# Kernel tuning notes

Measured on AMD Instinct MI355X. Metric: run time of the kernel, lower is better.

Reference implementation:

```python
import jax, jax.numpy as jnp
import numpy as np

DIM = 256; H = 64; W = 64; NH = 8; NL = 1; NP = 8; HD = DIM // NH
B = 4


def _bilinear(img, grid):
    """torch.grid_sample(mode='bilinear', padding='zeros', align_corners=False).
    img: [C, Hl, Wl]; grid: [N, P, 2] normalized xy in [-1, 1]. Returns [C, N, P]."""
    Hl, Wl = img.shape[1], img.shape[2]
    x = (grid[..., 0] + 1.0) * (Wl * 0.5) - 0.5
    y = (grid[..., 1] + 1.0) * (Hl * 0.5) - 0.5
    x0 = jnp.floor(x); y0 = jnp.floor(y)
    wx = x - x0; wy = y - y0

    def gather(xi, yi):
        valid = (xi >= 0) & (xi < Wl) & (yi >= 0) & (yi < Hl)
        xc = jnp.clip(xi, 0, Wl - 1).astype(jnp.int32)
        yc = jnp.clip(yi, 0, Hl - 1).astype(jnp.int32)
        return img[:, yc, xc] * valid.astype(img.dtype)[None]  # [C, N, P]

    v00 = gather(x0, y0); v01 = gather(x0 + 1, y0)
    v10 = gather(x0, y0 + 1); v11 = gather(x0 + 1, y0 + 1)
    top = v00 * (1.0 - wx) + v01 * wx
    bot = v10 * (1.0 - wx) + v11 * wx
    return top * (1.0 - wy) + bot * wy


def _msda(value, loc, att):
    """multi_scale_deformable_attn_pytorch.
    value: [b, nv, NH, HD]; loc: [b, nq, NH, NL, NP, 2] in [0,1]; att: [b, nq, NH, NL, NP]."""
    b, nv, _, _ = value.shape
    nq = loc.shape[1]
    grids = 2.0 * loc - 1.0
    bn = b * NH
    level_shapes = [(H, W)] * NL  # all levels share the single [H, W] grid here
    sampled_levels = []
    offset = 0
    for l, (Hl, Wl) in enumerate(level_shapes):
        vl = value[:, offset:offset + Hl * Wl]                     # [b, HW, NH, HD]
        offset += Hl * Wl
        vl = vl.transpose(0, 2, 3, 1).reshape(bn, HD, Hl, Wl)      # [b*NH, HD, Hl, Wl]
        gl = grids[:, :, :, l].transpose(0, 2, 1, 3, 4).reshape(bn, nq, NP, 2)
        sampled_levels.append(jax.vmap(_bilinear)(vl, gl))         # [b*NH, HD, nq, NP]
    sampled = jnp.stack(sampled_levels, axis=3)                    # [b*NH, HD, nq, NL, NP]
    w = att.transpose(0, 2, 1, 3, 4).reshape(bn, 1, nq, NL, NP)
    out = jnp.sum(sampled * w, axis=(3, 4))                        # [b*NH, HD, nq]
    return out.reshape(b, NH, HD, nq).transpose(0, 3, 1, 2).reshape(b, nq, NH * HD)


def _forward(query, value, W_loc, b_loc, W_att, b_att, W_val, b_val, W_out, b_out):
    b = query.shape[0]
    nq = H * W
    q = query.transpose(0, 2, 3, 1).reshape(b, nq, DIM)
    v = value.transpose(0, 2, 3, 1).reshape(b, nq, DIM)
    loc = (q @ W_loc.T + b_loc).reshape(b, nq, NH, NL, NP, 2)
    att = jax.nn.softmax((q @ W_att.T + b_att).reshape(b, nq, NH, NL * NP), axis=-1)
    att = att.reshape(b, nq, NH, NL, NP)
    v = (v @ W_val.T + b_val).reshape(b, nq, NH, HD)
    out = _msda(v, loc, att)                                       # [b, nq, DIM]
    return out @ W_out.T + b_out


def setup_inputs() -> dict:
    key = jax.random.key(0)
    ks = jax.random.split(key, 12)
    s = 0.02
    return {
        "query": jax.random.normal(ks[0], (B, DIM, H, W), jnp.float32),
        "value": jax.random.normal(ks[1], (B, DIM, H, W), jnp.float32),
        "W_loc": jax.random.normal(ks[2], (NH * NL * NP * 2, DIM), jnp.float32) * s,
        "b_loc": jax.random.normal(ks[3], (NH * NL * NP * 2,), jnp.float32) * s,
        "W_att": jax.random.normal(ks[4], (NH * NL * NP, DIM), jnp.float32) * s,
        "b_att": jax.random.normal(ks[5], (NH * NL * NP,), jnp.float32) * s,
        "W_val": jax.random.normal(ks[6], (DIM, DIM), jnp.float32) * s,
        "b_val": jax.random.normal(ks[7], (DIM,), jnp.float32) * s,
        "W_out": jax.random.normal(ks[8], (DIM, DIM), jnp.float32) * s,
        "b_out": jax.random.normal(ks[9], (DIM,), jnp.float32) * s,
    }


def reference(query, value, W_loc, b_loc, W_att, b_att, W_val, b_val, W_out, b_out):
    return _forward(query, value, W_loc, b_loc, W_att, b_att, W_val, b_val, W_out, b_out)
```

## Files before the change

### kernel.cpp

```cpp
#include <hip/hip_runtime.h>
#include <hip/hip_bf16.h>
#include <math.h>

#define NQ   4096
#define DIMC 256
#define NHC  8
#define NPC  8
#define HDC  32
#define HC   64
#define WC   64
#define BC   4
#define LSTR 40

typedef __bf16 bf16x8 __attribute__((ext_vector_type(8)));
typedef __attribute__((ext_vector_type(4))) float f4;
typedef __attribute__((ext_vector_type(8))) short s8v;

__device__ __forceinline__ ushort f2bf(float f) {
  __hip_bfloat16 h = __float2bfloat16(f);
  union { __hip_bfloat16 h; ushort u; } c; c.h = h; return c.u;
}
__device__ __forceinline__ float bfu2f(ushort u) {
  union { unsigned i; float f; } c; c.i = ((unsigned)u) << 16; return c.f;
}
__device__ __forceinline__ float bflo(unsigned u) {
  union { unsigned i; float f; } c; c.i = u << 16; return c.f;
}
__device__ __forceinline__ float bfhi(unsigned u) {
  union { unsigned i; float f; } c; c.i = u & 0xffff0000u; return c.f;
}

__global__ __launch_bounds__(256) void k_locatt(
    const float* __restrict__ query,
    const float* __restrict__ W_loc, const float* __restrict__ b_loc,
    const float* __restrict__ W_att, const float* __restrict__ b_att,
    float* __restrict__ loc, float* __restrict__ att) {
  __shared__ __align__(16) ushort Ah[64 * LSTR], Al[64 * LSTR];
  __shared__ __align__(16) ushort Wh[64 * LSTR], Wl[64 * LSTR];
  const int b = blockIdx.z, n0 = blockIdx.x * 64, o0 = blockIdx.y * 64;
  const int tid = threadIdx.x, lane = tid & 63, wid = tid >> 6;
  const int wn0 = (wid & 1) * 32, wo0 = (wid >> 1) * 32;
  const int am = lane & 15, kq = (lane >> 4) * 8;
  const int an = tid & 63, ak = (tid >> 6) * 8;
  const int wo = tid >> 2, wk = (tid & 3) * 8;
  const float* Xb = query + (size_t)b * DIMC * NQ + n0 + an;
  const int oo = o0 + wo;
  const float* Wrow = (oo < 128) ? (W_loc + (size_t)oo * DIMC)
                                 : (W_att + (size_t)(oo - 128) * DIMC);

  f4 acc[2][2];
#pragma unroll
  for (int mi = 0; mi < 2; ++mi) { acc[mi][0] = (f4)0.f; acc[mi][1] = (f4)0.f; }

  float ax[8];
  float4 wx0, wx1;
#pragma unroll
  for (int j = 0; j < 8; ++j) ax[j] = Xb[(size_t)(ak + j) * NQ];
  wx0 = *(const float4*)(Wrow + wk);
  wx1 = *(const float4*)(Wrow + wk + 4);

  for (int t = 0; t < 8; ++t) {
    __syncthreads();
    {
      union { ushort u[8]; s8v s; } ph, pl;
#pragma unroll
      for (int j = 0; j < 8; ++j) {
        ushort h = f2bf(ax[j]);
        ph.u[j] = h;
        pl.u[j] = f2bf(ax[j] - bfu2f(h));
      }
      *(s8v*)(&Ah[an * LSTR + ak]) = ph.s;
      *(s8v*)(&Al[an * LSTR + ak]) = pl.s;
      float wt[8] = {wx0.x, wx0.y, wx0.z, wx0.w, wx1.x, wx1.y, wx1.z, wx1.w};
      union { ushort u[8]; s8v s; } qh, ql;
#pragma unroll
      for (int j = 0; j < 8; ++j) {
        ushort h = f2bf(wt[j]);
        qh.u[j] = h;
        ql.u[j] = f2bf(wt[j] - bfu2f(h));
      }
      *(s8v*)(&Wh[wo * LSTR + wk]) = qh.s;
      *(s8v*)(&Wl[wo * LSTR + wk]) = ql.s;
    }
    if (t < 7) {
      const int k0 = (t + 1) * 32;
#pragma unroll
      for (int j = 0; j < 8; ++j) ax[j] = Xb[(size_t)(k0 + ak + j) * NQ];
      wx0 = *(const float4*)(Wrow + k0 + wk);
      wx1 = *(const float4*)(Wrow + k0 + wk + 4);
    }
    __syncthreads();
    bf16x8 ah[2], al[2], bh[2], bl[2];
#pragma unroll
    for (int mi = 0; mi < 2; ++mi) {
      ah[mi] = *(const bf16x8*)(&Ah[(wn0 + mi * 16 + am) * LSTR + kq]);
      al[mi] = *(const bf16x8*)(&Al[(wn0 + mi * 16 + am) * LSTR + kq]);
    }
#pragma unroll
    for (int oj = 0; oj < 2; ++oj) {
      bh[oj] = *(const bf16x8*)(&Wh[(wo0 + oj * 16 + am) * LSTR + kq]);
      bl[oj] = *(const bf16x8*)(&Wl[(wo0 + oj * 16 + am) * LSTR + kq]);
    }
#pragma unroll
    for (int mi = 0; mi < 2; ++mi)
#pragma unroll
      for (int oj = 0; oj < 2; ++oj) {
        acc[mi][oj] = __builtin_amdgcn_mfma_f32_16x16x32_bf16(ah[mi], bh[oj], acc[mi][oj], 0, 0, 0);
        acc[mi][oj] = __builtin_amdgcn_mfma_f32_16x16x32_bf16(al[mi], bh[oj], acc[mi][oj], 0, 0, 0);
        acc[mi][oj] = __builtin_amdgcn_mfma_f32_16x16x32_bf16(ah[mi], bl[oj], acc[mi][oj], 0, 0, 0);
      }
  }
  const bool isAtt = (o0 >= 128);
  float* dstBase = isAtt ? att : loc;
  const float* bias = isAtt ? b_att : b_loc;
  const int ostride = isAtt ? 64 : 128;
  const int ob = isAtt ? o0 - 128 : o0;
#pragma unroll
  for (int oj = 0; oj < 2; ++oj) {
    const int o = ob + wo0 + oj * 16 + am;
    const float bv = bias[o];
#pragma unroll
    for (int mi = 0; mi < 2; ++mi) {
      const int nb = n0 + wn0 + mi * 16 + (lane >> 4) * 4;
#pragma unroll
      for (int r = 0; r < 4; ++r)
        dstBase[((size_t)b * NQ + nb + r) * ostride + o] = acc[mi][oj][r] + bv;
    }
  }
}

__global__ __launch_bounds__(256) void k_vproj(
    const float* __restrict__ value, const float* __restrict__ W_val,
    const float* __restrict__ b_val, ushort* __restrict__ vproj) {
  __shared__ __align__(16) ushort As[64 * LSTR];
  __shared__ __align__(16) ushort Ws[64 * LSTR];
  const int b = blockIdx.z, n0 = blockIdx.x * 64, o0 = blockIdx.y * 64;
  const int tid = threadIdx.x, lane = tid & 63, wid = tid >> 6;
  const int wn0 = (wid & 1) * 32, wo0 = (wid >> 1) * 32;
  const int am = lane & 15, kq = (lane >> 4) * 8;
  const int an = tid & 63, ak = (tid >> 6) * 8;
  const int wo = tid >> 2, wk = (tid & 3) * 8;
  const float* Xb = value + (size_t)b * DIMC * NQ + n0 + an;
  const float* Wrow = W_val + (size_t)(o0 + wo) * DIMC;

  f4 acc[2][2];
#pragma unroll
  for (int mi = 0; mi < 2; ++mi) { acc[mi][0] = (f4)0.f; acc[mi][1] = (f4)0.f; }

  float ax[8];
  float4 wx0, wx1;
#pragma unroll
  for (int j = 0; j < 8; ++j) ax[j] = Xb[(size_t)(ak + j) * NQ];
  wx0 = *(const float4*)(Wrow + wk);
  wx1 = *(const float4*)(Wrow + wk + 4);

  for (int t = 0; t < 8; ++t) {
    __syncthreads();
    {
      union { ushort u[8]; s8v s; } pa;
#pragma unroll
      for (int j = 0; j < 8; ++j) pa.u[j] = f2bf(ax[j]);
      *(s8v*)(&As[an * LSTR + ak]) = pa.s;
      float wt[8] = {wx0.x, wx0.y, wx0.z, wx0.w, wx1.x, wx1.y, wx1.z, wx1.w};
      union { ushort u[8]; s8v s; } pw;
#pragma unroll
      for (int j = 0; j < 8; ++j) pw.u[j] = f2bf(wt[j]);
      *(s8v*)(&Ws[wo * LSTR + wk]) = pw.s;
    }
    if (t < 7) {
      const int k0 = (t + 1) * 32;
#pragma unroll
      for (int j = 0; j < 8; ++j) ax[j] = Xb[(size_t)(k0 + ak + j) * NQ];
      wx0 = *(const float4*)(Wrow + k0 + wk);
      wx1 = *(const float4*)(Wrow + k0 + wk + 4);
    }
    __syncthreads();
    bf16x8 af[2], bf[2];
#pragma unroll
    for (int mi = 0; mi < 2; ++mi)
      af[mi] = *(const bf16x8*)(&As[(wn0 + mi * 16 + am) * LSTR + kq]);
#pragma unroll
    for (int oj = 0; oj < 2; ++oj)
      bf[oj] = *(const bf16x8*)(&Ws[(wo0 + oj * 16 + am) * LSTR + kq]);
#pragma unroll
    for (int mi = 0; mi < 2; ++mi)
#pragma unroll
      for (int oj = 0; oj < 2; ++oj)
        acc[mi][oj] = __builtin_amdgcn_mfma_f32_16x16x32_bf16(af[mi], bf[oj], acc[mi][oj], 0, 0, 0);
  }
#pragma unroll
  for (int oj = 0; oj < 2; ++oj) {
    const int o = o0 + wo0 + oj * 16 + am;
    const int h = o >> 5, d = o & 31;
    const float bias = b_val[o];
    ushort* dst = vproj + ((size_t)(b * NHC + h) * NQ) * HDC + d;
#pragma unroll
    for (int mi = 0; mi < 2; ++mi) {
      const int nb = n0 + wn0 + mi * 16 + (lane >> 4) * 4;
#pragma unroll
      for (int r = 0; r < 4; ++r)
        dst[(size_t)(nb + r) * HDC] = f2bf(acc[mi][oj][r] + bias);
    }
  }
}

__global__ __launch_bounds__(256) void k_sample(
    const float* __restrict__ loc, const float* __restrict__ attL,
    const ushort* __restrict__ vproj, ushort* __restrict__ msda) {
  __shared__ float4 Lc[64][9];
  __shared__ int4   Lo[64][9];
  const int b = blockIdx.z, h = blockIdx.y;
  const int tid = threadIdx.x;
  const int n0 = blockIdx.x * 64;
#pragma unroll
  for (int it = 0; it < 2; ++it) {
    const int idx = it * 256 + tid;
    const int q = idx >> 3, p = idx & 7;
    const int n = n0 + q;
    const float lg = attL[((size_t)b * NQ + n) * 64 + h * 8 + p];
    float m = lg;
#pragma unroll
    for (int off = 1; off < 8; off <<= 1) m = fmaxf(m, __shfl_xor(m, off, 64));
    const float e = __expf(lg - m);
    float s = e;
#pragma unroll
    for (int off = 1; off < 8; off <<= 1) s += __shfl_xor(s, off, 64);
    const float w = e / s;
    const float2 xy = *(const float2*)(loc + ((size_t)b * NQ + n) * 128 + h * 16 + p * 2);
    const float x = xy.x * 64.0f - 0.5f;
    const float y = xy.y * 64.0f - 0.5f;
    const float x0f = floorf(x), y0f = floorf(y);
    const float wx = x - x0f, wy = y - y0f;
    const int x0 = (int)x0f, y0 = (int)y0f;
    const int x1 = x0 + 1, y1 = y0 + 1;
    const float fx0 = (x0 >= 0 && x0 < WC) ? 1.f : 0.f;
    const float fx1 = (x1 >= 0 && x1 < WC) ? 1.f : 0.f;
    const float fy0 = (y0 >= 0 && y0 < HC) ? 1.f : 0.f;
    const float fy1 = (y1 >= 0 && y1 < HC) ? 1.f : 0.f;
    const int cx0 = min(max(x0, 0), WC - 1), cx1 = min(max(x1, 0), WC - 1);
    const int cy0 = min(max(y0, 0), HC - 1), cy1 = min(max(y1, 0), HC - 1);
    float4 cf;
    cf.x = w * (1.f - wx) * (1.f - wy) * fx0 * fy0;
    cf.y = w * wx * (1.f - wy) * fx1 * fy0;
    cf.z = w * (1.f - wx) * wy * fx0 * fy1;
    cf.w = w * wx * wy * fx1 * fy1;
    int4 of;
    of.x = (cy0 * WC + cx0) * HDC; of.y = (cy0 * WC + cx1) * HDC;
    of.z = (cy1 * WC + cx0) * HDC; of.w = (cy1 * WC + cx1) * HDC;
    Lc[q][p] = cf; Lo[q][p] = of;
  }
  __syncthreads();
  const int q = tid >> 2, d8 = (tid & 3) * 8;
  const int n = n0 + q;
  const ushort* vb = vproj + (size_t)((b * NHC + h) * NQ) * HDC + d8;
  float a[8] = {};
#pragma unroll
  for (int p = 0; p < 8; ++p) {
    const int4 of = Lo[q][p];
    const float4 cf = Lc[q][p];
    const uint4 u00 = *(const uint4*)(vb + of.x);
    const uint4 u01 = *(const uint4*)(vb + of.y);
    const uint4 u10 = *(const uint4*)(vb + of.z);
    const uint4 u11 = *(const uint4*)(vb + of.w);
    const unsigned c00[4] = {u00.x, u00.y, u00.z, u00.w};
    const unsigned c01[4] = {u01.x, u01.y, u01.z, u01.w};
    const unsigned c10[4] = {u10.x, u10.y, u10.z, u10.w};
    const unsigned c11[4] = {u11.x, u11.y, u11.z, u11.w};
#pragma unroll
    for (int j = 0; j < 4; ++j) {
      a[2 * j]     += cf.x * bflo(c00[j]) + cf.y * bflo(c01[j]) + cf.z * bflo(c10[j]) + cf.w * bflo(c11[j]);
      a[2 * j + 1] += cf.x * bfhi(c00[j]) + cf.y * bfhi(c01[j]) + cf.z * bfhi(c10[j]) + cf.w * bfhi(c11[j]);
    }
  }
  union { ushort u[8]; s8v s; } r;
#pragma unroll
  for (int j = 0; j < 8; ++j) r.u[j] = f2bf(a[j]);
  *(s8v*)(msda + ((size_t)b * NQ + n) * DIMC + h * HDC + d8) = r.s;
}

__global__ __launch_bounds__(256) void k_out(
    const ushort* __restrict__ msda, const float* __restrict__ W_out,
    const float* __restrict__ b_out, float* __restrict__ out) {
  __shared__ __align__(16) ushort As[64 * LSTR];
  __shared__ __align__(16) ushort Ws[64 * LSTR];
  const int b = blockIdx.z, n0 = blockIdx.x * 64, o0 = blockIdx.y * 64;
  const int tid = threadIdx.x, lane = tid & 63, wid = tid >> 6;
  const int wn0 = (wid & 1) * 32, wo0 = (wid >> 1) * 32;
  const int am = lane & 15, kq = (lane >> 4) * 8;
  const int ar = tid >> 2, akq = (tid & 3) * 8;
  const int wo = tid >> 2, wk = (tid & 3) * 8;
  const ushort* Ab = msda + ((size_t)b * NQ + n0 + ar) * DIMC + akq;
  const float* Wrow = W_out + (size_t)(o0 + wo) * DIMC;

  f4 acc[2][2];
#pragma unroll
  for (int mi = 0; mi < 2; ++mi) { acc[mi][0] = (f4)0.f; acc[mi][1] = (f4)0.f; }

  s8v aval = *(const s8v*)(Ab);
  float4 wx0 = *(const float4*)(Wrow + wk);
  float4 wx1 = *(const float4*)(Wrow + wk + 4);

  for (int t = 0; t < 8; ++t) {
    __syncthreads();
    *(s8v*)(&As[ar * LSTR + akq]) = aval;
    {
      float wt[8] = {wx0.x, wx0.y, wx0.z, wx0.w, wx1.x, wx1.y, wx1.z, wx1.w};
      union { ushort u[8]; s8v s; } pw;
#pragma unroll
      for (int j = 0; j < 8; ++j) pw.u[j] = f2bf(wt[j]);
      *(s8v*)(&Ws[wo * LSTR + wk]) = pw.s;
    }
    if (t < 7) {
      const int k0 = (t + 1) * 32;
      aval = *(const s8v*)(Ab + k0);
      wx0 = *(const float4*)(Wrow + k0 + wk);
      wx1 = *(const float4*)(Wrow + k0 + wk + 4);
    }
    __syncthreads();
    bf16x8 af[2], bf[2];
#pragma unroll
    for (int mi = 0; mi < 2; ++mi)
      af[mi] = *(const bf16x8*)(&As[(wn0 + mi * 16 + am) * LSTR + kq]);
#pragma unroll
    for (int oj = 0; oj < 2; ++oj)
      bf[oj] = *(const bf16x8*)(&Ws[(wo0 + oj * 16 + am) * LSTR + kq]);
#pragma unroll
    for (int mi = 0; mi < 2; ++mi)
#pragma unroll
      for (int oj = 0; oj < 2; ++oj)
        acc[mi][oj] = __builtin_amdgcn_mfma_f32_16x16x32_bf16(af[mi], bf[oj], acc[mi][oj], 0, 0, 0);
  }
#pragma unroll
  for (int oj = 0; oj < 2; ++oj) {
    const int o = o0 + wo0 + oj * 16 + am;
    const float bias = b_out[o];
#pragma unroll
    for (int mi = 0; mi < 2; ++mi) {
      const int nb = n0 + wn0 + mi * 16 + (lane >> 4) * 4;
#pragma unroll
      for (int r = 0; r < 4; ++r)
        out[((size_t)b * NQ + nb + r) * DIMC + o] = acc[mi][oj][r] + bias;
    }
  }
}

extern "C" void kernel_launch(void* const* d_in, const int* in_sizes, int n_in,
                              void* d_out, int out_size, void* d_ws, size_t ws_size,
                              hipStream_t stream) {
  const float* query = (const float*)d_in[0];
  const float* value = (const float*)d_in[1];
  const float* W_loc = (const float*)d_in[2];
  const float* b_loc = (const float*)d_in[3];
  const float* W_att = (const float*)d_in[4];
  const float* b_att = (const float*)d_in[5];
  const float* W_val = (const float*)d_in[6];
  const float* b_val = (const float*)d_in[7];
  const float* W_out = (const float*)d_in[8];
  const float* b_out = (const float*)d_in[9];
  float* out = (float*)d_out;

  float* ws = (float*)d_ws;
  float* loc    = ws;
  float* att    = loc + (size_t)BC * NQ * 128;
  ushort* vproj = (ushort*)(att + (size_t)BC * NQ * 64);
  ushort* msda  = vproj + (size_t)BC * NHC * NQ * HDC;

  dim3 blk(256);
  k_locatt<<<dim3(NQ / 64, 3, BC), blk, 0, stream>>>(query, W_loc, b_loc, W_att, b_att, loc, att);
  k_vproj <<<dim3(NQ / 64, 4, BC), blk, 0, stream>>>(value, W_val, b_val, vproj);
  k_sample<<<dim3(NQ / 64, NHC, BC), blk, 0, stream>>>(loc, att, vproj, msda);
  k_out   <<<dim3(NQ / 64, 4, BC), blk, 0, stream>>>(msda, W_out, b_out, out);
}
```

Baseline: 130.7 us.

## Merge loc/att and value projections into one launch; pre-convert W_out to bf16

The loc/att projection and value projection kernels are merged into a single launch whose grid y-dimension selects the branch. An extra slice of blocks converts W_out to bf16 into workspace. k_out now stages the whole 64x256 msda tile into shared memory once and reads the bf16 weights directly from global memory, with no per-step syncs. This removes one launch and the repeated fp32-to-bf16 weight conversion in k_out, at the cost of larger shared memory per block in k_out and uncoalesced global weight reads that depend on the cache.

```diff
diff --git a/kernel.cpp b/kernel.cpp
--- a/kernel.cpp
+++ b/kernel.cpp
@@ -11,6 +11,7 @@
 #define WC   64
 #define BC   4
 #define LSTR 40
+#define KSTR 280
 
 typedef __bf16 bf16x8 __attribute__((ext_vector_type(8)));
 typedef __attribute__((ext_vector_type(4))) float f4;
@@ -30,176 +31,181 @@
   union { unsigned i; float f; } c; c.i = u & 0xffff0000u; return c.f;
 }
 
-__global__ __launch_bounds__(256) void k_locatt(
-    const float* __restrict__ query,
+__global__ __launch_bounds__(256) void k_proj(
+    const float* __restrict__ query, const float* __restrict__ value,
     const float* __restrict__ W_loc, const float* __restrict__ b_loc,
     const float* __restrict__ W_att, const float* __restrict__ b_att,
-    float* __restrict__ loc, float* __restrict__ att) {
-  __shared__ __align__(16) ushort Ah[64 * LSTR], Al[64 * LSTR];
-  __shared__ __align__(16) ushort Wh[64 * LSTR], Wl[64 * LSTR];
-  const int b = blockIdx.z, n0 = blockIdx.x * 64, o0 = blockIdx.y * 64;
-  const int tid = threadIdx.x, lane = tid & 63, wid = tid >> 6;
+    const float* __restrict__ W_val, const float* __restrict__ b_val,
+    const float* __restrict__ W_out,
+    float* __restrict__ loc, float* __restrict__ att,
+    ushort* __restrict__ vproj, ushort* __restrict__ woutb) {
+  __shared__ __align__(16) ushort smem[4 * 64 * LSTR];
+  const int oy = blockIdx.y;
+  const int tid = threadIdx.x;
+
+  if (oy == 7) {
+    const int idx = (blockIdx.z * 64 + blockIdx.x) * 256 + tid;
+    woutb[idx] = f2bf(W_out[idx]);
+    return;
+  }
+
+  const int b = blockIdx.z, n0 = blockIdx.x * 64;
+  const int lane = tid & 63, wid = tid >> 6;
   const int wn0 = (wid & 1) * 32, wo0 = (wid >> 1) * 32;
   const int am = lane & 15, kq = (lane >> 4) * 8;
   const int an = tid & 63, ak = (tid >> 6) * 8;
   const int wo = tid >> 2, wk = (tid & 3) * 8;
-  const float* Xb = query + (size_t)b * DIMC * NQ + n0 + an;
-  const int oo = o0 + wo;
-  const float* Wrow = (oo < 128) ? (W_loc + (size_t)oo * DIMC)
-                                 : (W_att + (size_t)(oo - 128) * DIMC);
 
   f4 acc[2][2];
 #pragma unroll
   for (int mi = 0; mi < 2; ++mi) { acc[mi][0] = (f4)0.f; acc[mi][1] = (f4)0.f; }
 
-  float ax[8];
-  float4 wx0, wx1;
-#pragma unroll
-  for (int j = 0; j < 8; ++j) ax[j] = Xb[(size_t)(ak + j) * NQ];
-  wx0 = *(const float4*)(Wrow + wk);
-  wx1 = *(const float4*)(Wrow + wk + 4);
-
-  for (int t = 0; t < 8; ++t) {
-    __syncthreads();
-    {
-      union { ushort u[8]; s8v s; } ph, pl;
-#pragma unroll
-      for (int j = 0; j < 8; ++j) {
-        ushort h = f2bf(ax[j]);
-        ph.u[j] = h;
-        pl.u[j] = f2bf(ax[j] - bfu2f(h));
-      }
-      *(s8v*)(&Ah[an * LSTR + ak]) = ph.s;
-      *(s8v*)(&Al[an * LSTR + ak]) = pl.s;
-      float wt[8] = {wx0.x, wx0.y, wx0.z, wx0.w, wx1.x, wx1.y, wx1.z, wx1.w};
-      union { ushort u[8]; s8v s; } qh, ql;
-#pragma unroll
-      for (int j = 0; j < 8; ++j) {
-        ushort h = f2bf(wt[j]);
-        qh.u[j] = h;
-        ql.u[j] = f2bf(wt[j] - bfu2f(h));
-      }
-      *(s8v*)(&Wh[wo * LSTR + wk]) = qh.s;
-      *(s8v*)(&Wl[wo * LSTR + wk]) = ql.s;
-    }
-    if (t < 7) {
-      const int k0 = (t + 1) * 32;
-#pragma unroll
-      for (int j = 0; j < 8; ++j) ax[j] = Xb[(size_t)(k0 + ak + j) * NQ];
-      wx0 = *(const float4*)(Wrow + k0 + wk);
-      wx1 = *(const float4*)(Wrow + k0 + wk + 4);
-    }
-    __syncthreads();
-    bf16x8 ah[2], al[2], bh[2], bl[2];
-#pragma unroll
-    for (int mi = 0; mi < 2; ++mi) {
-      ah[mi] = *(const bf16x8*)(&Ah[(wn0 + mi * 16 + am) * LSTR + kq]);
-      al[mi] = *(const bf16x8*)(&Al[(wn0 + mi * 16 + am) * LSTR + kq]);
-    }
+  if (oy < 3) {
+    ushort* Ah = smem;
+    ushort* Al = smem + 64 * LSTR;
+    ushort* Wh = smem + 2 * 64 * LSTR;
+    ushort* Wl = smem + 3 * 64 * LSTR;
+    const int o0 = oy * 64;
+    const float* Xb = query + (size_t)b * DIMC * NQ + n0 + an;
+    const int oo = o0 + wo;
+    const float* Wrow = (oo < 128) ? (W_loc + (size_t)oo * DIMC)
+                                   : (W_att + (size_t)(oo - 128) * DIMC);
+    float ax[8];
+    float4 wx0, wx1;
+#pragma unroll
+    for (int j = 0; j < 8; ++j) ax[j] = Xb[(size_t)(ak + j) * NQ];
+    wx0 = *(const float4*)(Wrow + wk);
+    wx1 = *(const float4*)(Wrow + wk + 4);
+
+    for (int t = 0; t < 8; ++t) {
+      __syncthreads();
+      {
+        union { ushort u[8]; s8v s; } ph, pl;
+#pragma unroll
+        for (int j = 0; j < 8; ++j) {
+          ushort h = f2bf(ax[j]);
+          ph.u[j] = h;
+          pl.u[j] = f2bf(ax[j] - bfu2f(h));
+        }
+        *(s8v*)(&Ah[an * LSTR + ak]) = ph.s;
+        *(s8v*)(&Al[an * LSTR + ak]) = pl.s;
+        float wt[8] = {wx0.x, wx0.y, wx0.z, wx0.w, wx1.x, wx1.y, wx1.z, wx1.w};
+        union { ushort u[8]; s8v s; } qh, ql;
+#pragma unroll
+        for (int j = 0; j < 8; ++j) {
+          ushort h = f2bf(wt[j]);
+          qh.u[j] = h;
+          ql.u[j] = f2bf(wt[j] - bfu2f(h));
+        }
+        *(s8v*)(&Wh[wo * LSTR + wk]) = qh.s;
+        *(s8v*)(&Wl[wo * LSTR + wk]) = ql.s;
+      }
+      if (t < 7) {
+        const int k0 = (t + 1) * 32;
+#pragma unroll
+        for (int j = 0; j < 8; ++j) ax[j] = Xb[(size_t)(k0 + ak + j) * NQ];
+        wx0 = *(const float4*)(Wrow + k0 + wk);
+        wx1 = *(const float4*)(Wrow + k0 + wk + 4);
+      }
+      __syncthreads();
+      bf16x8 ah[2], al[2], bh[2], bl[2];
+#pragma unroll
+      for (int mi = 0; mi < 2; ++mi) {
+        ah[mi] = *(const bf16x8*)(&Ah[(wn0 + mi * 16 + am) * LSTR + kq]);
+        al[mi] = *(const bf16x8*)(&Al[(wn0 + mi * 16 + am) * LSTR + kq]);
+      }
+#pragma unroll
+      for (int oj = 0; oj < 2; ++oj) {
+        bh[oj] = *(const bf16x8*)(&Wh[(wo0 + oj * 16 + am) * LSTR + kq]);
+        bl[oj] = *(const bf16x8*)(&Wl[(wo0 + oj * 16 + am) * LSTR + kq]);
+      }
+#pragma unroll
+      for (int mi = 0; mi < 2; ++mi)
+#pragma unroll
+        for (int oj = 0; oj < 2; ++oj) {
+          acc[mi][oj] = __builtin_amdgcn_mfma_f32_16x16x32_bf16(ah[mi], bh[oj], acc[mi][oj], 0, 0, 0);
+          acc[mi][oj] = __builtin_amdgcn_mfma_f32_16x16x32_bf16(al[mi], bh[oj], acc[mi][oj], 0, 0, 0);
+          acc[mi][oj] = __builtin_amdgcn_mfma_f32_16x16x32_bf16(ah[mi], bl[oj], acc[mi][oj], 0, 0, 0);
+        }
+    }
+    const bool isAtt = (o0 >= 128);
+    float* dstBase = isAtt ? att : loc;
+    const float* bias = isAtt ? b_att : b_loc;
+    const int ostride = isAtt ? 64 : 128;
+    const int ob = isAtt ? o0 - 128 : o0;
 #pragma unroll
     for (int oj = 0; oj < 2; ++oj) {
-      bh[oj] = *(const bf16x8*)(&Wh[(wo0 + oj * 16 + am) * LSTR + kq]);
-      bl[oj] = *(const bf16x8*)(&Wl[(wo0 + oj * 16 + am) * LSTR + kq]);
-    }
-#pragma unroll
-    for (int mi = 0; mi < 2; ++mi)
-#pragma unroll
-      for (int oj = 0; oj < 2; ++oj) {
-        acc[mi][oj] = __builtin_amdgcn_mfma_f32_16x16x32_bf16(ah[mi], bh[oj], acc[mi][oj], 0, 0, 0);
-        acc[mi][oj] = __builtin_amdgcn_mfma_f32_16x16x32_bf16(al[mi], bh[oj], acc[mi][oj], 0, 0, 0);
-        acc[mi][oj] = __builtin_amdgcn_mfma_f32_16x16x32_bf16(ah[mi], bl[oj], acc[mi][oj], 0, 0, 0);
-      }
-  }
-  const bool isAtt = (o0 >= 128);
-  float* dstBase = isAtt ? att : loc;
-  const float* bias = isAtt ? b_att : b_loc;
-  const int ostride = isAtt ? 64 : 128;
-  const int ob = isAtt ? o0 - 128 : o0;
-#pragma unroll
-  for (int oj = 0; oj < 2; ++oj) {
-    const int o = ob + wo0 + oj * 16 + am;
-    const float bv = bias[o];
-#pragma unroll
-    for (int mi = 0; mi < 2; ++mi) {
-      const int nb = n0 + wn0 + mi * 16 + (lane >> 4) * 4;
-#pragma unroll
-      for (int r = 0; r < 4; ++r)
-        dstBase[((size_t)b * NQ + nb + r) * ostride + o] = acc[mi][oj][r] + bv;
-    }
-  }
-}
-
-__global__ __launch_bounds__(256) void k_vproj(
-    const float* __restrict__ value, const float* __restrict__ W_val,
-    const float* __restrict__ b_val, ushort* __restrict__ vproj) {
-  __shared__ __align__(16) ushort As[64 * LSTR];
-  __shared__ __align__(16) ushort Ws[64 * LSTR];
-  const int b = blockIdx.z, n0 = blockIdx.x * 64, o0 = blockIdx.y * 64;
-  const int tid = threadIdx.x, lane = tid & 63, wid = tid >> 6;
-  const int wn0 = (wid & 1) * 32, wo0 = (wid >> 1) * 32;
-  const int am = lane & 15, kq = (lane >> 4) * 8;
-  const int an = tid & 63, ak = (tid >> 6) * 8;
-  const int wo = tid >> 2, wk = (tid & 3) * 8;
-  const float* Xb = value + (size_t)b * DIMC * NQ + n0 + an;
-  const float* Wrow = W_val + (size_t)(o0 + wo) * DIMC;
-
-  f4 acc[2][2];
-#pragma unroll
-  for (int mi = 0; mi < 2; ++mi) { acc[mi][0] = (f4)0.f; acc[mi][1] = (f4)0.f; }
-
-  float ax[8];
-  float4 wx0, wx1;
-#pragma unroll
-  for (int j = 0; j < 8; ++j) ax[j] = Xb[(size_t)(ak + j) * NQ];
-  wx0 = *(const float4*)(Wrow + wk);
-  wx1 = *(const float4*)(Wrow + wk + 4);
-
-  for (int t = 0; t < 8; ++t) {
-    __syncthreads();
-    {
-      union { ushort u[8]; s8v s; } pa;
-#pragma unroll
-      for (int j = 0; j < 8; ++j) pa.u[j] = f2bf(ax[j]);
-      *(s8v*)(&As[an * LSTR + ak]) = pa.s;
-      float wt[8] = {wx0.x, wx0.y, wx0.z, wx0.w, wx1.x, wx1.y, wx1.z, wx1.w};
-      union { ushort u[8]; s8v s; } pw;
-#pragma unroll
-      for (int j = 0; j < 8; ++j) pw.u[j] = f2bf(wt[j]);
-      *(s8v*)(&Ws[wo * LSTR + wk]) = pw.s;
-    }
-    if (t < 7) {
-      const int k0 = (t + 1) * 32;
-#pragma unroll
-      for (int j = 0; j < 8; ++j) ax[j] = Xb[(size_t)(k0 + ak + j) * NQ];
-      wx0 = *(const float4*)(Wrow + k0 + wk);
-      wx1 = *(const float4*)(Wrow + k0 + wk + 4);
-    }
-    __syncthreads();
-    bf16x8 af[2], bf[2];
-#pragma unroll
-    for (int mi = 0; mi < 2; ++mi)
-      af[mi] = *(const bf16x8*)(&As[(wn0 + mi * 16 + am) * LSTR + kq]);
-#pragma unroll
-    for (int oj = 0; oj < 2; ++oj)
-      bf[oj] = *(const bf16x8*)(&Ws[(wo0 + oj * 16 + am) * LSTR + kq]);
-#pragma unroll
-    for (int mi = 0; mi < 2; ++mi)
+      const int o = ob + wo0 + oj * 16 + am;
+      const float bv = bias[o];
+#pragma unroll
+      for (int mi = 0; mi < 2; ++mi) {
+        const int nb = n0 + wn0 + mi * 16 + (lane >> 4) * 4;
+#pragma unroll
+        for (int r = 0; r < 4; ++r)
+          dstBase[((size_t)b * NQ + nb + r) * ostride + o] = acc[mi][oj][r] + bv;
+      }
+    }
+  } else {
+    ushort* As = smem;
+    ushort* Ws = smem + 64 * LSTR;
+    const int o0 = (oy - 3) * 64;
+    const float* Xb = value + (size_t)b * DIMC * NQ + n0 + an;
+    const float* Wrow = W_val + (size_t)(o0 + wo) * DIMC;
+
+    float ax[8];
+    float4 wx0, wx1;
+#pragma unroll
+    for (int j = 0; j < 8; ++j) ax[j] = Xb[(size_t)(ak + j) * NQ];
+    wx0 = *(const float4*)(Wrow + wk);
+    wx1 = *(const float4*)(Wrow + wk + 4);
+
+    for (int t = 0; t < 8; ++t) {
+      __syncthreads();
+      {
+        union { ushort u[8]; s8v s; } pa;
+#pragma unroll
+        for (int j = 0; j < 8; ++j) pa.u[j] = f2bf(ax[j]);
+        *(s8v*)(&As[an * LSTR + ak]) = pa.s;
+        float wt[8] = {wx0.x, wx0.y, wx0.z, wx0.w, wx1.x, wx1.y, wx1.z, wx1.w};
+        union { ushort u[8]; s8v s; } pw;
+#pragma unroll
+        for (int j = 0; j < 8; ++j) pw.u[j] = f2bf(wt[j]);
+        *(s8v*)(&Ws[wo * LSTR + wk]) = pw.s;
+      }
+      if (t < 7) {
+        const int k0 = (t + 1) * 32;
+#pragma unroll
+        for (int j = 0; j < 8; ++j) ax[j] = Xb[(size_t)(k0 + ak + j) * NQ];
+        wx0 = *(const float4*)(Wrow + k0 + wk);
+        wx1 = *(const float4*)(Wrow + k0 + wk + 4);
+      }
+      __syncthreads();
+      bf16x8 af[2], bf[2];
+#pragma unroll
+      for (int mi = 0; mi < 2; ++mi)
+        af[mi] = *(const bf16x8*)(&As[(wn0 + mi * 16 + am) * LSTR + kq]);
 #pragma unroll
       for (int oj = 0; oj < 2; ++oj)
-        acc[mi][oj] = __builtin_amdgcn_mfma_f32_16x16x32_bf16(af[mi], bf[oj], acc[mi][oj], 0, 0, 0);
-  }
-#pragma unroll
-  for (int oj = 0; oj < 2; ++oj) {
-    const int o = o0 + wo0 + oj * 16 + am;
-    const int h = o >> 5, d = o & 31;
-    const float bias = b_val[o];
-    ushort* dst = vproj + ((size_t)(b * NHC + h) * NQ) * HDC + d;
-#pragma unroll
-    for (int mi = 0; mi < 2; ++mi) {
-      const int nb = n0 + wn0 + mi * 16 + (lane >> 4) * 4;
-#pragma unroll
-      for (int r = 0; r < 4; ++r)
-        dst[(size_t)(nb + r) * HDC] = f2bf(acc[mi][oj][r] + bias);
+        bf[oj] = *(const bf16x8*)(&Ws[(wo0 + oj * 16 + am) * LSTR + kq]);
+#pragma unroll
+      for (int mi = 0; mi < 2; ++mi)
+#pragma unroll
+        for (int oj = 0; oj < 2; ++oj)
+          acc[mi][oj] = __builtin_amdgcn_mfma_f32_16x16x32_bf16(af[mi], bf[oj], acc[mi][oj], 0, 0, 0);
+    }
+#pragma unroll
+    for (int oj = 0; oj < 2; ++oj) {
+      const int o = o0 + wo0 + oj * 16 + am;
+      const int h = o >> 5, d = o & 31;
+      const float bias = b_val[o];
+      ushort* dst = vproj + ((size_t)(b * NHC + h) * NQ) * HDC + d;
+#pragma unroll
+      for (int mi = 0; mi < 2; ++mi) {
+        const int nb = n0 + wn0 + mi * 16 + (lane >> 4) * 4;
+#pragma unroll
+        for (int r = 0; r < 4; ++r)
+          dst[(size_t)(nb + r) * HDC] = f2bf(acc[mi][oj][r] + bias);
+      }
     }
   }
 }
@@ -279,56 +285,39 @@
 }
 
 __global__ __launch_bounds__(256) void k_out(
-    const ushort* __restrict__ msda, const float* __restrict__ W_out,
+    const ushort* __restrict__ msda, const ushort* __restrict__ Wb,
     const float* __restrict__ b_out, float* __restrict__ out) {
-  __shared__ __align__(16) ushort As[64 * LSTR];
-  __shared__ __align__(16) ushort Ws[64 * LSTR];
+  __shared__ __align__(16) ushort As[64 * KSTR];
   const int b = blockIdx.z, n0 = blockIdx.x * 64, o0 = blockIdx.y * 64;
   const int tid = threadIdx.x, lane = tid & 63, wid = tid >> 6;
   const int wn0 = (wid & 1) * 32, wo0 = (wid >> 1) * 32;
   const int am = lane & 15, kq = (lane >> 4) * 8;
-  const int ar = tid >> 2, akq = (tid & 3) * 8;
-  const int wo = tid >> 2, wk = (tid & 3) * 8;
-  const ushort* Ab = msda + ((size_t)b * NQ + n0 + ar) * DIMC + akq;
-  const float* Wrow = W_out + (size_t)(o0 + wo) * DIMC;
+
+  const int an = tid >> 2, akc = (tid & 3) * 64;
+  const ushort* Ap = msda + ((size_t)b * NQ + n0 + an) * DIMC + akc;
+  s8v av[8];
+#pragma unroll
+  for (int j = 0; j < 8; ++j) av[j] = *(const s8v*)(Ap + j * 8);
+#pragma unroll
+  for (int j = 0; j < 8; ++j) *(s8v*)(&As[an * KSTR + akc + j * 8]) = av[j];
 
   f4 acc[2][2];
 #pragma unroll
   for (int mi = 0; mi < 2; ++mi) { acc[mi][0] = (f4)0.f; acc[mi][1] = (f4)0.f; }
 
-  s8v aval = *(const s8v*)(Ab);
-  float4 wx0 = *(const float4*)(Wrow + wk);
-  float4 wx1 = *(const float4*)(Wrow + wk + 4);
-
+  const ushort* W0 = Wb + (size_t)(o0 + wo0 + am) * DIMC + kq;
+  const ushort* W1 = Wb + (size_t)(o0 + wo0 + 16 + am) * DIMC + kq;
+  __syncthreads();
+#pragma unroll
   for (int t = 0; t < 8; ++t) {
-    __syncthreads();
-    *(s8v*)(&As[ar * LSTR + akq]) = aval;
-    {
-      float wt[8] = {wx0.x, wx0.y, wx0.z, wx0.w, wx1.x, wx1.y, wx1.z, wx1.w};
-      union { ushort u[8]; s8v s; } pw;
-#pragma unroll
-      for (int j = 0; j < 8; ++j) pw.u[j] = f2bf(wt[j]);
-      *(s8v*)(&Ws[wo * LSTR + wk]) = pw.s;
-    }
-    if (t < 7) {
-      const int k0 = (t + 1) * 32;
-      aval = *(const s8v*)(Ab + k0);
-      wx0 = *(const float4*)(Wrow + k0 + wk);
-      wx1 = *(const float4*)(Wrow + k0 + wk + 4);
-    }
-    __syncthreads();
-    bf16x8 af[2], bf[2];
-#pragma unroll
-    for (int mi = 0; mi < 2; ++mi)
-      af[mi] = *(const bf16x8*)(&As[(wn0 + mi * 16 + am) * LSTR + kq]);
-#pragma unroll
-    for (int oj = 0; oj < 2; ++oj)
-      bf[oj] = *(const bf16x8*)(&Ws[(wo0 + oj * 16 + am) * LSTR + kq]);
-#pragma unroll
-    for (int mi = 0; mi < 2; ++mi)
-#pragma unroll
-      for (int oj = 0; oj < 2; ++oj)
-        acc[mi][oj] = __builtin_amdgcn_mfma_f32_16x16x32_bf16(af[mi], bf[oj], acc[mi][oj], 0, 0, 0);
+    bf16x8 af0 = *(const bf16x8*)(&As[(wn0 + am) * KSTR + t * 32 + kq]);
+    bf16x8 af1 = *(const bf16x8*)(&As[(wn0 + 16 + am) * KSTR + t * 32 + kq]);
+    bf16x8 bf0 = *(const bf16x8*)(W0 + t * 32);
+    bf16x8 bf1 = *(const bf16x8*)(W1 + t * 32);
+    acc[0][0] = __builtin_amdgcn_mfma_f32_16x16x32_bf16(af0, bf0, acc[0][0], 0, 0, 0);
+    acc[1][0] = __builtin_amdgcn_mfma_f32_16x16x32_bf16(af1, bf0, acc[1][0], 0, 0, 0);
+    acc[0][1] = __builtin_amdgcn_mfma_f32_16x16x32_bf16(af0, bf1, acc[0][1], 0, 0, 0);
+    acc[1][1] = __builtin_amdgcn_mfma_f32_16x16x32_bf16(af1, bf1, acc[1][1], 0, 0, 0);
   }
 #pragma unroll
   for (int oj = 0; oj < 2; ++oj) {
@@ -364,10 +353,11 @@
   float* att    = loc + (size_t)BC * NQ * 128;
   ushort* vproj = (ushort*)(att + (size_t)BC * NQ * 64);
   ushort* msda  = vproj + (size_t)BC * NHC * NQ * HDC;
+  ushort* woutb = msda + (size_t)BC * NQ * DIMC;
 
   dim3 blk(256);
-  k_locatt<<<dim3(NQ / 64, 3, BC), blk, 0, stream>>>(query, W_loc, b_loc, W_att, b_att, loc, att);
-  k_vproj <<<dim3(NQ / 64, 4, BC), blk, 0, stream>>>(value, W_val, b_val, vproj);
+  k_proj  <<<dim3(NQ / 64, 8, BC), blk, 0, stream>>>(query, value, W_loc, b_loc,
+             W_att, b_att, W_val, b_val, W_out, loc, att, vproj, woutb);
   k_sample<<<dim3(NQ / 64, NHC, BC), blk, 0, stream>>>(loc, att, vproj, msda);
-  k_out   <<<dim3(NQ / 64, 4, BC), blk, 0, stream>>>(msda, W_out, b_out, out);
-}
+  k_out   <<<dim3(NQ / 64, 4, BC), blk, 0, stream>>>(msda, woutb, b_out, out);
+}
```

Result: slower. 135.2 us (+3.4%).
